# Performance work log

Measured on AMD Instinct MI355X. Metric: run time of the kernel, lower is better.

Reference implementation:

```python
import jax, jax.numpy as jnp
import numpy as np

B, D_IN, D_OUT = 8192, 4096, 2048

def setup_inputs() -> dict:
    key = jax.random.key(0)
    k1, k2, k3 = jax.random.split(key, 3)
    inputs = jax.random.normal(k1, (B, D_IN), dtype=jnp.float32)
    # xavier-uniform kernel
    limit = float(np.sqrt(6.0 / (D_IN + D_OUT)))
    kernel = jax.random.uniform(k2, (D_IN, D_OUT), dtype=jnp.float32, minval=-limit, maxval=limit)
    bias = jnp.zeros((D_OUT,), dtype=jnp.float32)
    map_ = jax.random.bernoulli(k3, p=0.1, shape=(D_IN, D_OUT)).astype(jnp.float32)
    return {"inputs": inputs, "kernel": kernel, "bias": bias, "map": map_}

def reference(inputs, kernel, bias, map):
    # SparseTF: mask the weight in place, then dense GEMM + bias
    masked_kernel = kernel * map            # [D_IN, D_OUT]
    out = inputs @ masked_kernel + bias     # [B, D_OUT]
    return out
```

## Files before the change

kernel.cpp:

```cpp
#include <hip/hip_runtime.h>

#define BB   8192
#define DIN  4096
#define DOUT 2048

typedef unsigned short ushort_t;
typedef __attribute__((ext_vector_type(8))) short bf16x8;
typedef __attribute__((ext_vector_type(4))) float f32x4;

__device__ inline ushort_t f2bf(float f) {
    union { float f; unsigned u; } v; v.f = f;
    unsigned u = v.u;
    return (ushort_t)((u + 0x7fffu + ((u >> 16) & 1u)) >> 16);
}

#define GLOAD16(g, s)                                                        \
    __builtin_amdgcn_global_load_lds(                                        \
        (const __attribute__((address_space(1))) void*)(g),                  \
        (__attribute__((address_space(3))) void*)(s), 16, 0, 0)

#define FENCE() asm volatile("" ::: "memory")
#define BAR()   do { FENCE(); __builtin_amdgcn_s_barrier(); FENCE(); } while (0)
#define VMCNT(n) asm volatile("s_waitcnt vmcnt(" #n ")" ::: "memory")

struct __align__(8) us4 { ushort_t x, y, z, w; };

__global__ __launch_bounds__(256) void convA(const float4* __restrict__ in,
                                             us4* __restrict__ out, int n4) {
    int i = blockIdx.x * blockDim.x + threadIdx.x;
    int stride = gridDim.x * blockDim.x;
    for (; i < n4; i += stride) {
        float4 v = in[i];
        us4 o;
        o.x = f2bf(v.x); o.y = f2bf(v.y); o.z = f2bf(v.z); o.w = f2bf(v.w);
        out[i] = o;
    }
}

__global__ __launch_bounds__(256) void maskT(const float* __restrict__ Kn,
                                             const float* __restrict__ Mp,
                                             ushort_t* __restrict__ WT) {
    __shared__ ushort_t t[32][33];
    const int n0 = blockIdx.x * 32;
    const int k0 = blockIdx.y * 32;
    const int tx = threadIdx.x, ty = threadIdx.y;
    #pragma unroll
    for (int i = ty; i < 32; i += 8) {
        size_t idx = (size_t)(k0 + i) * DOUT + (n0 + tx);
        t[i][tx] = f2bf(Kn[idx] * Mp[idx]);
    }
    __syncthreads();
    #pragma unroll
    for (int i = ty; i < 32; i += 8) {
        WT[(size_t)(n0 + i) * DIN + (k0 + tx)] = t[tx][i];
    }
}

__global__ __launch_bounds__(512) void gemm8(const ushort_t* __restrict__ A,
                                             const ushort_t* __restrict__ BT,
                                             const float* __restrict__ bias,
                                             float* __restrict__ C) {
    constexpr int K = DIN, N = DOUT;
    constexpr int NT = K / 64;
    extern __shared__ char sb[];

    const int tid  = threadIdx.x;
    const int lane = tid & 63;
    const int w    = tid >> 6;
    const int wr   = w >> 2;
    const int wcn  = w & 3;
    const int l15  = lane & 15;

    const int orig = blockIdx.y * 8 + blockIdx.x;
    const int swz  = (orig & 7) * 32 + (orig >> 3);
    const int n0   = (swz & 7) * 256;
    const int m0   = (swz >> 3) * 256;

    const int srow = lane >> 3;
    const int scol = ((lane & 7) ^ srow) * 8;
    const ushort_t* Ab = A  + (size_t)(m0 + srow) * K + scol;
    const ushort_t* Bb = BT + (size_t)(n0 + srow) * K + scol;

    auto stgA = [&](int buf, int kt, int h, int c) {
        GLOAD16(Ab + (size_t)(h * 128 + c * 8) * K + kt * 64,
                sb + buf * 65536 + h * 16384 + c * 1024);
    };
    auto stgB = [&](int buf, int kt, int h, int c) {
        GLOAD16(Bb + (size_t)(h * 128 + c * 8) * K + kt * 64,
                sb + buf * 65536 + 32768 + h * 16384 + c * 1024);
    };

    const int fxor = (l15 & 7) << 4;
    const int kq   = (lane >> 4) * 16;

    f32x4 acc[8][4] = {};
    bf16x8 bf[4][2];

    stgB(0, 0, 0, w); stgB(0, 0, 0, 8 + w);
    stgB(0, 0, 1, w); stgB(0, 0, 1, 8 + w);
    stgA(0, 0, 0, w); stgA(0, 0, 1, w);
    stgA(0, 0, 0, 8 + w); stgA(0, 0, 1, 8 + w);
    VMCNT(2);
    BAR();

    for (int t = 0; t < NT; ++t) {
        const int  cur = t & 1;
        const int  nxt = cur ^ 1;
        const bool pf  = (t + 1 < NT);
        const char* Abase = sb + cur * 65536 + wr * 16384;
        const char* Bbase = sb + cur * 65536 + 32768 + (wcn >> 1) * 16384 + (wcn & 1) * 8192;

        #pragma unroll
        for (int q = 0; q < 4; ++q) {
            bf16x8 af[2][2];
            #pragma unroll
            for (int mm = 0; mm < 2; ++mm)
                #pragma unroll
                for (int ks = 0; ks < 2; ++ks)
                    af[mm][ks] = *(const bf16x8*)(Abase + (2 * q + mm) * 2048 + l15 * 128 +
                                                  ((ks * 64 + kq) ^ fxor));
            if (q == 0) {
                #pragma unroll
                for (int n = 0; n < 4; ++n)
                    #pragma unroll
                    for (int ks = 0; ks < 2; ++ks)
                        bf[n][ks] = *(const bf16x8*)(Bbase + n * 2048 + l15 * 128 +
                                                     ((ks * 64 + kq) ^ fxor));
            }
            if (pf) {
                if      (q == 0) { stgB(nxt, t + 1, 0, w); stgB(nxt, t + 1, 0, 8 + w); }
                else if (q == 1) { stgB(nxt, t + 1, 1, w); stgB(nxt, t + 1, 1, 8 + w); }
                else if (q == 2) { stgA(nxt, t + 1, 0, w); stgA(nxt, t + 1, 1, w); }
                else             { stgA(nxt, t + 1, 0, 8 + w); stgA(nxt, t + 1, 1, 8 + w); }
            }
            BAR();
            __builtin_amdgcn_s_setprio(1);
            #pragma unroll
            for (int ks = 0; ks < 2; ++ks)
                #pragma unroll
                for (int mm = 0; mm < 2; ++mm)
                    #pragma unroll
                    for (int n = 0; n < 4; ++n)
                        acc[2 * q + mm][n] = __builtin_amdgcn_mfma_f32_16x16x32_bf16(
                            af[mm][ks], bf[n][ks], acc[2 * q + mm][n], 0, 0, 0);
            __builtin_amdgcn_s_setprio(0);
            if (q == 1) {
                if (pf) { VMCNT(4); }
                else    { VMCNT(0); }
            }
            if (q == 3 && pf) { VMCNT(2); }
            BAR();
        }
    }

    #pragma unroll
    for (int n = 0; n < 4; ++n) {
        const int col = n0 + wcn * 64 + n * 16 + l15;
        const float bv = bias[col];
        #pragma unroll
        for (int m = 0; m < 8; ++m) {
            const int r0 = m0 + wr * 128 + m * 16 + (lane >> 4) * 4;
            #pragma unroll
            for (int j = 0; j < 4; ++j)
                C[(size_t)(r0 + j) * N + col] = acc[m][n][j] + bv;
        }
    }
}

__global__ __launch_bounds__(1024) void gemm_fb(const float* __restrict__ A,
                                                const float* __restrict__ Kn,
                                                const float* __restrict__ Mp,
                                                const float* __restrict__ bias,
                                                float* __restrict__ C) {
    __shared__ float As[32][33];
    __shared__ float Bs[32][33];
    const int tx = threadIdx.x, ty = threadIdx.y;
    const int row = blockIdx.y * 32 + ty;
    const int col = blockIdx.x * 32 + tx;
    float acc = 0.f;
    for (int kt = 0; kt < DIN; kt += 32) {
        As[ty][tx] = A[(size_t)row * DIN + kt + tx];
        size_t bidx = (size_t)(kt + ty) * DOUT + col;
        Bs[ty][tx] = Kn[bidx] * Mp[bidx];
        __syncthreads();
        #pragma unroll
        for (int kk = 0; kk < 32; ++kk)
            acc += As[ty][kk] * Bs[kk][tx];
        __syncthreads();
    }
    C[(size_t)row * DOUT + col] = acc + bias[col];
}

extern "C" void kernel_launch(void* const* d_in, const int* in_sizes, int n_in,
                              void* d_out, int out_size, void* d_ws, size_t ws_size,
                              hipStream_t stream) {
    const float* inputs = (const float*)d_in[0];
    const float* kernel = (const float*)d_in[1];
    const float* bias   = (const float*)d_in[2];
    const float* map    = (const float*)d_in[3];
    float* out = (float*)d_out;

    const size_t abytes = (size_t)BB * DIN * sizeof(ushort_t);
    const size_t wbytes = (size_t)DIN * DOUT * sizeof(ushort_t);

    if (ws_size >= abytes + wbytes) {
        ushort_t* Abf = (ushort_t*)d_ws;
        ushort_t* WT  = (ushort_t*)((char*)d_ws + abytes);

        static bool attr_set = false;
        if (!attr_set) {
            hipFuncSetAttribute((const void*)gemm8,
                                hipFuncAttributeMaxDynamicSharedMemorySize, 131072);
            attr_set = true;
        }

        convA<<<2048, 256, 0, stream>>>((const float4*)inputs, (us4*)Abf,
                                        (int)((size_t)BB * DIN / 4));
        maskT<<<dim3(DOUT / 32, DIN / 32), dim3(32, 8), 0, stream>>>(kernel, map, WT);
        gemm8<<<dim3(DOUT / 256, BB / 256), 512, 131072, stream>>>(Abf, WT, bias, out);
    } else {
        gemm_fb<<<dim3(DOUT / 32, BB / 32), dim3(32, 32), 0, stream>>>(inputs, kernel, map,
                                                                       bias, out);
    }
}
```

Before: 162.8 us.

## Fuse fp32-to-bf16 conversion of A into GEMM via register-staged loads

Removes the separate conversion kernel for the input matrix. The GEMM instead loads fp32 A tiles into registers, converts them with packed bf16 conversion instructions, and writes them to swizzled LDS. The k-loop is reordered so each quarter iteration handles half the M rows for one k-slice, and all B prefetches are issued up front. This saves a full read/write pass over A but doubles the A bytes each GEMM block fetches, and adds register pressure and explicit waits.

```diff
diff --git a/kernel.cpp b/kernel.cpp
--- a/kernel.cpp
+++ b/kernel.cpp
@@ -22,20 +22,7 @@
 #define FENCE() asm volatile("" ::: "memory")
 #define BAR()   do { FENCE(); __builtin_amdgcn_s_barrier(); FENCE(); } while (0)
 #define VMCNT(n) asm volatile("s_waitcnt vmcnt(" #n ")" ::: "memory")
-
-struct __align__(8) us4 { ushort_t x, y, z, w; };
-
-__global__ __launch_bounds__(256) void convA(const float4* __restrict__ in,
-                                             us4* __restrict__ out, int n4) {
-    int i = blockIdx.x * blockDim.x + threadIdx.x;
-    int stride = gridDim.x * blockDim.x;
-    for (; i < n4; i += stride) {
-        float4 v = in[i];
-        us4 o;
-        o.x = f2bf(v.x); o.y = f2bf(v.y); o.z = f2bf(v.z); o.w = f2bf(v.w);
-        out[i] = o;
-    }
-}
+#define LGKM0()  asm volatile("s_waitcnt lgkmcnt(0)" ::: "memory")
 
 __global__ __launch_bounds__(256) void maskT(const float* __restrict__ Kn,
                                              const float* __restrict__ Mp,
@@ -56,7 +43,7 @@
     }
 }
 
-__global__ __launch_bounds__(512) void gemm8(const ushort_t* __restrict__ A,
+__global__ __launch_bounds__(512) void gemm8(const float* __restrict__ A,
                                              const ushort_t* __restrict__ BT,
                                              const float* __restrict__ bias,
                                              float* __restrict__ C) {
@@ -78,29 +65,41 @@
 
     const int srow = lane >> 3;
     const int scol = ((lane & 7) ^ srow) * 8;
-    const ushort_t* Ab = A  + (size_t)(m0 + srow) * K + scol;
     const ushort_t* Bb = BT + (size_t)(n0 + srow) * K + scol;
-
-    auto stgA = [&](int buf, int kt, int h, int c) {
-        GLOAD16(Ab + (size_t)(h * 128 + c * 8) * K + kt * 64,
-                sb + buf * 65536 + h * 16384 + c * 1024);
-    };
     auto stgB = [&](int buf, int kt, int h, int c) {
         GLOAD16(Bb + (size_t)(h * 128 + c * 8) * K + kt * 64,
                 sb + buf * 65536 + 32768 + h * 16384 + c * 1024);
     };
 
+    const float* Aft = A + (size_t)(m0 + (tid >> 4)) * K + (tid & 15) * 4;
+    float4 apf[4];
+    auto issueA = [&](int kt, int hf) {
+        #pragma unroll
+        for (int j = 0; j < 4; ++j)
+            apf[j] = *(const float4*)(Aft + (size_t)(hf * 128 + j * 32) * K + kt * 64);
+    };
+    const int awoff = (tid >> 4) * 128 + (((tid & 15) * 8) ^ (((tid >> 4) & 7) << 4));
+    auto writeA = [&](int buf, int hf) {
+        #pragma unroll
+        for (int j = 0; j < 4; ++j) {
+            uint2 p;
+            asm("v_cvt_pk_bf16_f32 %0, %1, %2" : "=v"(p.x) : "v"(apf[j].x), "v"(apf[j].y));
+            asm("v_cvt_pk_bf16_f32 %0, %1, %2" : "=v"(p.y) : "v"(apf[j].z), "v"(apf[j].w));
+            *(uint2*)(sb + buf * 65536 + hf * 16384 + j * 4096 + awoff) = p;
+        }
+    };
+
     const int fxor = (l15 & 7) << 4;
     const int kq   = (lane >> 4) * 16;
 
     f32x4 acc[8][4] = {};
-    bf16x8 bf[4][2];
-
+    bf16x8 bfk[4];
+
+    issueA(0, 0); VMCNT(0); writeA(0, 0);
+    issueA(0, 1); VMCNT(0); writeA(0, 1);
     stgB(0, 0, 0, w); stgB(0, 0, 0, 8 + w);
     stgB(0, 0, 1, w); stgB(0, 0, 1, 8 + w);
-    stgA(0, 0, 0, w); stgA(0, 0, 1, w);
-    stgA(0, 0, 0, 8 + w); stgA(0, 0, 1, 8 + w);
-    VMCNT(2);
+    VMCNT(0); LGKM0();
     BAR();
 
     for (int t = 0; t < NT; ++t) {
@@ -108,47 +107,47 @@
         const int  nxt = cur ^ 1;
         const bool pf  = (t + 1 < NT);
         const char* Abase = sb + cur * 65536 + wr * 16384;
-        const char* Bbase = sb + cur * 65536 + 32768 + (wcn >> 1) * 16384 + (wcn & 1) * 8192;
+        const char* Bbase = sb + cur * 65536 + 32768 + wcn * 8192;
 
         #pragma unroll
         for (int q = 0; q < 4; ++q) {
-            bf16x8 af[2][2];
+            const int mh = q & 1;
+            const int ks = q >> 1;
+            bf16x8 af[4];
             #pragma unroll
-            for (int mm = 0; mm < 2; ++mm)
-                #pragma unroll
-                for (int ks = 0; ks < 2; ++ks)
-                    af[mm][ks] = *(const bf16x8*)(Abase + (2 * q + mm) * 2048 + l15 * 128 +
-                                                  ((ks * 64 + kq) ^ fxor));
-            if (q == 0) {
+            for (int mm = 0; mm < 4; ++mm)
+                af[mm] = *(const bf16x8*)(Abase + (mh * 4 + mm) * 2048 + l15 * 128 +
+                                          ((ks * 64 + kq) ^ fxor));
+            if (mh == 0) {
                 #pragma unroll
                 for (int n = 0; n < 4; ++n)
-                    #pragma unroll
-                    for (int ks = 0; ks < 2; ++ks)
-                        bf[n][ks] = *(const bf16x8*)(Bbase + n * 2048 + l15 * 128 +
-                                                     ((ks * 64 + kq) ^ fxor));
-            }
-            if (pf) {
-                if      (q == 0) { stgB(nxt, t + 1, 0, w); stgB(nxt, t + 1, 0, 8 + w); }
-                else if (q == 1) { stgB(nxt, t + 1, 1, w); stgB(nxt, t + 1, 1, 8 + w); }
-                else if (q == 2) { stgA(nxt, t + 1, 0, w); stgA(nxt, t + 1, 1, w); }
-                else             { stgA(nxt, t + 1, 0, 8 + w); stgA(nxt, t + 1, 1, 8 + w); }
+                    bfk[n] = *(const bf16x8*)(Bbase + n * 2048 + l15 * 128 +
+                                              ((ks * 64 + kq) ^ fxor));
+            }
+            if (q == 0 && pf) {
+                issueA(t + 1, 0);
+                stgB(nxt, t + 1, 0, w); stgB(nxt, t + 1, 0, 8 + w);
+                stgB(nxt, t + 1, 1, w); stgB(nxt, t + 1, 1, 8 + w);
             }
             BAR();
             __builtin_amdgcn_s_setprio(1);
             #pragma unroll
-            for (int ks = 0; ks < 2; ++ks)
+            for (int mm = 0; mm < 4; ++mm)
                 #pragma unroll
-                for (int mm = 0; mm < 2; ++mm)
-                    #pragma unroll
-                    for (int n = 0; n < 4; ++n)
-                        acc[2 * q + mm][n] = __builtin_amdgcn_mfma_f32_16x16x32_bf16(
-                            af[mm][ks], bf[n][ks], acc[2 * q + mm][n], 0, 0, 0);
+                for (int n = 0; n < 4; ++n)
+                    acc[mh * 4 + mm][n] = __builtin_amdgcn_mfma_f32_16x16x32_bf16(
+                        af[mm], bfk[n], acc[mh * 4 + mm][n], 0, 0, 0);
             __builtin_amdgcn_s_setprio(0);
-            if (q == 1) {
-                if (pf) { VMCNT(4); }
-                else    { VMCNT(0); }
-            }
-            if (q == 3 && pf) { VMCNT(2); }
+            if (q == 2 && pf) {
+                VMCNT(4);
+                writeA(nxt, 0);
+                issueA(t + 1, 1);
+            }
+            if (q == 3 && pf) {
+                VMCNT(0);
+                writeA(nxt, 1);
+                LGKM0();
+            }
             BAR();
         }
     }
@@ -200,12 +199,10 @@
     const float* map    = (const float*)d_in[3];
     float* out = (float*)d_out;
 
-    const size_t abytes = (size_t)BB * DIN * sizeof(ushort_t);
     const size_t wbytes = (size_t)DIN * DOUT * sizeof(ushort_t);
 
-    if (ws_size >= abytes + wbytes) {
-        ushort_t* Abf = (ushort_t*)d_ws;
-        ushort_t* WT  = (ushort_t*)((char*)d_ws + abytes);
+    if (ws_size >= wbytes) {
+        ushort_t* WT = (ushort_t*)d_ws;
 
         static bool attr_set = false;
         if (!attr_set) {
@@ -214,10 +211,8 @@
             attr_set = true;
         }
 
-        convA<<<2048, 256, 0, stream>>>((const float4*)inputs, (us4*)Abf,
-                                        (int)((size_t)BB * DIN / 4));
         maskT<<<dim3(DOUT / 32, DIN / 32), dim3(32, 8), 0, stream>>>(kernel, map, WT);
-        gemm8<<<dim3(DOUT / 256, BB / 256), 512, 131072, stream>>>(Abf, WT, bias, out);
+        gemm8<<<dim3(DOUT / 256, BB / 256), 512, 131072, stream>>>(inputs, WT, bias, out);
     } else {
         gemm_fb<<<dim3(DOUT / 32, BB / 32), dim3(32, 32), 0, stream>>>(inputs, kernel, map,
                                                                        bias, out);
```

After: 190.3 us. 1.17x slower.
